# Optimization experiments

Measured on AMD Instinct MI355X. Metric: run time of the kernel, lower is better.

The kernel has to match this reference:

```python
import jax, jax.numpy as jnp
import numpy as np

B, T, S, D, VOCAB = 16, 64, 128, 512, 32000


def setup_inputs():
    key = jax.random.key(0)
    ks = jax.random.split(key, 20)
    w = lambda i, shape: jax.random.normal(ks[i], shape, dtype=jnp.float32) * 0.05
    return {
        'words': jax.random.randint(ks[0], (B, T), 0, VOCAB),
        'encoder_output': jax.random.normal(ks[1], (B, S, D), dtype=jnp.float32),
        'pre_h': jax.random.normal(ks[2], (B, D), dtype=jnp.float32),
        'cell': jax.random.normal(ks[3], (B, D), dtype=jnp.float32),
        'emb': w(4, (VOCAB, D)),
        'W_ih': w(5, (4 * D, D)), 'W_hh': w(6, (4 * D, D)),
        'b_ih': w(7, (4 * D,)), 'b_hh': w(8, (4 * D,)),
        'Wh_w': w(9, (D, D)),
        'Ws_w': w(10, (D, D)), 'Ws_b': w(11, (D,)),
        'vt_w': w(12, (D,)),
        'V_w': w(13, (D, 2 * D)), 'V_b': w(14, (D,)),
        'Vp_w': w(15, (VOCAB, D)), 'Vp_b': w(16, (VOCAB,)),
    }


def lstm(xs, h0, c0, W_ih, W_hh, b_ih, b_hh):
    # xs: [T, B, D]; PyTorch LSTM gate order: i, f, g, o
    def step(carry, x_t):
        h, c = carry
        g = x_t @ W_ih.T + b_ih + h @ W_hh.T + b_hh
        i, f, gg, o = jnp.split(g, 4, axis=-1)
        c = jax.nn.sigmoid(f) * c + jax.nn.sigmoid(i) * jnp.tanh(gg)
        h = jax.nn.sigmoid(o) * jnp.tanh(c)
        return (h, c), h
    _, hs = jax.lax.scan(step, (h0, c0), xs)
    return hs


def reference(words, encoder_output, pre_h, cell, emb, W_ih, W_hh, b_ih, b_hh,
              Wh_w, Ws_w, Ws_b, vt_w, V_w, V_b, Vp_w, Vp_b):
    x = emb[words]                                   # [B, T, D]
    hs = lstm(x.transpose(1, 0, 2), pre_h, cell, W_ih, W_hh, b_ih, b_hh)
    out = hs.transpose(1, 0, 2)                      # [B, T, D] decoder states
    wh = encoder_output @ Wh_w.T                     # [B, S, D]
    ws = out @ Ws_w.T + Ws_b                         # [B, T, D]
    # Bahdanau additive attention scores e[b,s,t] = v_t . tanh(wh[b,s] + ws[b,t])
    e = jnp.einsum('bstd,d->bst', jnp.tanh(wh[:, :, None, :] + ws[:, None, :, :]), vt_w)
    a = jax.nn.softmax(e, axis=1)                    # softmax over source positions
    context = jnp.einsum('bst,bsd->btd', a, encoder_output)
    cat = jnp.concatenate([context, out], axis=-1)   # [B, T, 2D]
    return (cat @ V_w.T + V_b) @ Vp_w.T + Vp_b       # [B, T, VOCAB]
```

## Files before the change

### kernel.cpp

```cpp
#include <hip/hip_runtime.h>

#define DEV __device__ __forceinline__

typedef float f32x4 __attribute__((ext_vector_type(4)));
typedef short s16x8 __attribute__((ext_vector_type(8)));
typedef unsigned short u16;
typedef u16 u16x4 __attribute__((ext_vector_type(4)));
typedef u16 u16x8 __attribute__((ext_vector_type(8)));
typedef unsigned int u32x4 __attribute__((ext_vector_type(4)));

constexpr int Bb = 16, Tt = 64, Ss = 128, Dd = 512, Vv = 32000, FD = 2048;

DEV u16 f2bf(float x) {
  unsigned u = __builtin_bit_cast(unsigned, x);
  u = u + 0x7fffu + ((u >> 16) & 1u);
  return (u16)(u >> 16);
}
DEV float bf2f(u16 h) { unsigned u = ((unsigned)h) << 16; return __builtin_bit_cast(float, u); }
DEV float sigm(float x) { return 1.f / (1.f + __expf(-x)); }
DEV float ftanh(float x) {
  x = fminf(15.f, fmaxf(-15.f, x));
  float e = __expf(2.f * x);
  return (e - 1.f) / (e + 1.f);
}

DEV void cvt_plain_one(const float* __restrict__ in, u16* __restrict__ out, int i) {
  float4 v = reinterpret_cast<const float4*>(in)[i];
  u16x4 o;
  o.x = f2bf(v.x); o.y = f2bf(v.y); o.z = f2bf(v.z); o.w = f2bf(v.w);
  reinterpret_cast<u16x4*>(out)[i] = o;
}

DEV void cvt_split_one(const float* __restrict__ in, u16* __restrict__ hi,
                       u16* __restrict__ lo, int i) {
  float4 v = reinterpret_cast<const float4*>(in)[i];
  u16x4 oh, ol;
  float vv[4] = {v.x, v.y, v.z, v.w};
#pragma unroll
  for (int j = 0; j < 4; ++j) {
    u16 h = f2bf(vv[j]);
    oh[j] = h;
    ol[j] = f2bf(vv[j] - bf2f(h));
  }
  reinterpret_cast<u16x4*>(hi)[i] = oh;
  reinterpret_cast<u16x4*>(lo)[i] = ol;
}

__global__ void k_pre(const int* __restrict__ words, const float* __restrict__ emb,
                      u16* __restrict__ xb,
                      const float* __restrict__ pre, unsigned* __restrict__ hp0,
                      const float* __restrict__ bi, const float* __restrict__ bh,
                      float* __restrict__ bsum,
                      const float* __restrict__ Wih, u16* __restrict__ Wih_bf,
                      const float* __restrict__ enc, u16* __restrict__ ench,
                      u16* __restrict__ encl,
                      const float* __restrict__ Whw, u16* __restrict__ whh,
                      u16* __restrict__ whl) {
  int blk = blockIdx.x, tid = threadIdx.x;
  if (blk < Bb * Tt) {
    int row = words[blk];
    int d = tid * 2;
    float2 v = *reinterpret_cast<const float2*>(&emb[(size_t)row * Dd + d]);
    xb[(size_t)blk * Dd + d] = f2bf(v.x);
    xb[(size_t)blk * Dd + d + 1] = f2bf(v.y);
  } else if (blk < Bb * Tt + 32) {
    int i = (blk - Bb * Tt) * 256 + tid;
    float v = pre[i];
    u16 h = f2bf(v);
    u16 l = f2bf(v - bf2f(h));
    hp0[i] = (unsigned)h | ((unsigned)l << 16);
  } else if (blk < Bb * Tt + 40) {
    int i = (blk - Bb * Tt - 32) * 256 + tid;
    bsum[i] = bi[i] + bh[i];
  } else {
    const int n0 = FD * Dd / 4, n1 = Bb * Ss * Dd / 4, n2 = Dd * Dd / 4;
    int total = n0 + n1 + n2;
    int i = (blk - (Bb * Tt + 40)) * 256 + tid;
    int st = 256 * 256;
    for (; i < total; i += st) {
      if (i < n0) cvt_plain_one(Wih, Wih_bf, i);
      else if (i < n0 + n1) cvt_split_one(enc, ench, encl, i - n0);
      else cvt_split_one(Whw, whh, whl, i - n0 - n1);
    }
  }
}

template <bool BIAS, bool OUTBF, int TERMS>
DEV void gemm_body(u16* ls, int tile, int tid,
                   const u16* __restrict__ A, const u16* __restrict__ Al,
                   const u16* __restrict__ Bm, const u16* __restrict__ Bl,
                   float* __restrict__ Cf, u16* __restrict__ Cb,
                   const float* __restrict__ bias, int M, int N, int K) {
  u16* lsA = ls;
  u16* lsB = ls + 128 * 32;
  u16* lsAl = ls + 2 * 128 * 32;
  u16* lsBl = ls + 3 * 128 * 32;
  const int mt = M >> 7;
  const int tm = (tile % mt) << 7;
  const int tn = (tile / mt) << 7;
  const int wave = tid >> 6, lane = tid & 63;
  const int wr = wave >> 1, wc = wave & 1;
  f32x4 acc[4][4];
#pragma unroll
  for (int i = 0; i < 4; ++i)
#pragma unroll
    for (int j = 0; j < 4; ++j) acc[i][j] = (f32x4){0.f, 0.f, 0.f, 0.f};

  const int lrow = lane >> 2;
  const int lk = (lane & 3) << 3;
  const int fr = lane & 15, fk = (lane >> 4) << 3;

  for (int k0 = 0; k0 < K; k0 += 32) {
#pragma unroll
    for (int r = 0; r < 2; ++r) {
      int rowA = r * 64 + wave * 16;
      size_t goffA = (size_t)(tm + rowA + lrow) * K + k0 + lk;
      size_t goffB = (size_t)(tn + rowA + lrow) * K + k0 + lk;
      __builtin_amdgcn_global_load_lds((const __attribute__((address_space(1))) void*)(A + goffA),
                                       (__attribute__((address_space(3))) void*)&lsA[rowA * 32],
                                       16, 0, 0);
      __builtin_amdgcn_global_load_lds((const __attribute__((address_space(1))) void*)(Bm + goffB),
                                       (__attribute__((address_space(3))) void*)&lsB[rowA * 32],
                                       16, 0, 0);
      if constexpr (TERMS == 3) {
        __builtin_amdgcn_global_load_lds((const __attribute__((address_space(1))) void*)(Al + goffA),
                                         (__attribute__((address_space(3))) void*)&lsAl[rowA * 32],
                                         16, 0, 0);
        __builtin_amdgcn_global_load_lds((const __attribute__((address_space(1))) void*)(Bl + goffB),
                                         (__attribute__((address_space(3))) void*)&lsBl[rowA * 32],
                                         16, 0, 0);
      }
    }
    __syncthreads();
    s16x8 av[4], bv[4];
#pragma unroll
    for (int mi = 0; mi < 4; ++mi)
      av[mi] = *reinterpret_cast<const s16x8*>(&lsA[(wr * 64 + mi * 16 + fr) * 32 + fk]);
#pragma unroll
    for (int ni = 0; ni < 4; ++ni)
      bv[ni] = *reinterpret_cast<const s16x8*>(&lsB[(wc * 64 + ni * 16 + fr) * 32 + fk]);
    if constexpr (TERMS == 3) {
      s16x8 avl[4], bvl[4];
#pragma unroll
      for (int mi = 0; mi < 4; ++mi)
        avl[mi] = *reinterpret_cast<const s16x8*>(&lsAl[(wr * 64 + mi * 16 + fr) * 32 + fk]);
#pragma unroll
      for (int ni = 0; ni < 4; ++ni)
        bvl[ni] = *reinterpret_cast<const s16x8*>(&lsBl[(wc * 64 + ni * 16 + fr) * 32 + fk]);
#pragma unroll
      for (int mi = 0; mi < 4; ++mi)
#pragma unroll
        for (int ni = 0; ni < 4; ++ni) {
          acc[mi][ni] = __builtin_amdgcn_mfma_f32_16x16x32_bf16(av[mi], bv[ni], acc[mi][ni], 0, 0, 0);
          acc[mi][ni] = __builtin_amdgcn_mfma_f32_16x16x32_bf16(av[mi], bvl[ni], acc[mi][ni], 0, 0, 0);
          acc[mi][ni] = __builtin_amdgcn_mfma_f32_16x16x32_bf16(avl[mi], bv[ni], acc[mi][ni], 0, 0, 0);
        }
    } else {
#pragma unroll
      for (int mi = 0; mi < 4; ++mi)
#pragma unroll
        for (int ni = 0; ni < 4; ++ni)
          acc[mi][ni] = __builtin_amdgcn_mfma_f32_16x16x32_bf16(av[mi], bv[ni], acc[mi][ni], 0, 0, 0);
    }
    __syncthreads();
  }

  const int fm = (lane >> 4) << 2;
#pragma unroll
  for (int ni = 0; ni < 4; ++ni) {
    int col = tn + wc * 64 + ni * 16 + fr;
    float badd = 0.f;
    if constexpr (BIAS) badd = bias[col];
#pragma unroll
    for (int mi = 0; mi < 4; ++mi) {
#pragma unroll
      for (int r = 0; r < 4; ++r) {
        int row = tm + wr * 64 + mi * 16 + fm + r;
        size_t idx = (size_t)row * N + col;
        float v = acc[mi][ni][r] + badd;
        if constexpr (OUTBF) Cb[idx] = f2bf(v);
        else Cf[idx] = v;
      }
    }
  }
}

template <bool BIAS, bool OUTBF, int TERMS>
__global__ __launch_bounds__(256) void k_gemm(const u16* __restrict__ A,
                                              const u16* __restrict__ Al,
                                              const u16* __restrict__ Bm,
                                              const u16* __restrict__ Bl,
                                              float* __restrict__ Cf, u16* __restrict__ Cb,
                                              const float* __restrict__ bias,
                                              int M, int N, int K) {
  __shared__ u16 ls[4 * 128 * 32];
  gemm_body<BIAS, OUTBF, TERMS>(ls, blockIdx.x, threadIdx.x, A, Al, Bm, Bl, Cf, Cb, bias, M, N, K);
}

__global__ __launch_bounds__(256) void k_logits_sw(const u16* __restrict__ hmid,
                                                   const u16* __restrict__ Vp_bf,
                                                   const float* __restrict__ Vp_b,
                                                   float* __restrict__ outp) {
  __shared__ u16 ls[4 * 128 * 32];
  const int id = blockIdx.x;
  const int n = (id & 7) + 8 * (id >> 6);
  const int m = (id >> 3) & 7;
  if (n >= 250) return;
  gemm_body<true, false, 1>(ls, n * 8 + m, threadIdx.x, hmid, nullptr, Vp_bf, nullptr,
                            outp, nullptr, Vp_b, 1024, 32000, 512);
}

DEV void lstm_body(int w, int tid, float* gls,
                   const float* __restrict__ xg, const float* __restrict__ Whh,
                   const float* __restrict__ cell, unsigned* __restrict__ hpack,
                   u16* __restrict__ out_hi, u16* __restrict__ out_lo,
                   int* __restrict__ flags) {
  const int gi = tid >> 6, lane = tid & 63;
  const int ds0 = w << 4;
  float (*g_lds)[16][16] = (float(*)[16][16])gls;

  const int fr = lane & 15;
  const int fkb = (lane >> 4) << 3;

  s16x8 whi[16], wlo[16];
  {
    const float* wrow = Whh + (size_t)(gi * Dd + ds0 + fr) * Dd;
#pragma unroll
    for (int kc = 0; kc < 16; ++kc) {
      int k = kc * 32 + fkb;
      float4 a = *reinterpret_cast<const float4*>(&wrow[k]);
      float4 b = *reinterpret_cast<const float4*>(&wrow[k + 4]);
      float vv[8] = {a.x, a.y, a.z, a.w, b.x, b.y, b.z, b.w};
#pragma unroll
      for (int j = 0; j < 8; ++j) {
        u16 h = f2bf(vv[j]);
        whi[kc][j] = (short)h;
        wlo[kc][j] = (short)f2bf(vv[j] - bf2f(h));
      }
    }
  }

  const int ub = tid >> 4, ud = tid & 15;
  float c = cell[(size_t)ub * Dd + ds0 + ud];

  for (int t = 0; t < Tt; ++t) {
    float xgv[4];
#pragma unroll
    for (int r = 0; r < 4; ++r) {
      int bb = ((lane >> 4) << 2) + r;
      xgv[r] = xg[(size_t)(bb * Tt + t) * FD + gi * Dd + ds0 + fr];
    }
#pragma unroll
    for (int r = 0; r < 4; ++r) asm volatile("" ::"v"(xgv[r]));

    if (t > 0) {
      if (gi == 0) {
        if (lane < 32 && lane != w) {
          while (__hip_atomic_load(&flags[lane * 32], __ATOMIC_RELAXED,
                                   __HIP_MEMORY_SCOPE_AGENT) < t) {}
          while (__hip_atomic_load(&flags[lane * 32], __ATOMIC_ACQUIRE,
                                   __HIP_MEMORY_SCOPE_AGENT) < t) {}
        }
        __builtin_amdgcn_sched_barrier(0);
      }
      __syncthreads();
    }

    const unsigned* hp = hpack + (size_t)t * (Bb * Dd) + (size_t)fr * Dd;
    f32x4 a0 = (f32x4){0.f, 0.f, 0.f, 0.f};
    f32x4 a1 = a0, a2 = a0;
#pragma unroll
    for (int kc = 0; kc < 16; ++kc) {
      int k = kc * 32 + fkb;
      u32x4 u0 = *reinterpret_cast<const u32x4*>(&hp[k]);
      u32x4 u1 = *reinterpret_cast<const u32x4*>(&hp[k + 4]);
      s16x8 ahi, alo;
#pragma unroll
      for (int j = 0; j < 4; ++j) {
        ahi[j] = (short)(u0[j] & 0xffffu); alo[j] = (short)(u0[j] >> 16);
        ahi[4 + j] = (short)(u1[j] & 0xffffu); alo[4 + j] = (short)(u1[j] >> 16);
      }
      a0 = __builtin_amdgcn_mfma_f32_16x16x32_bf16(ahi, whi[kc], a0, 0, 0, 0);
      a1 = __builtin_amdgcn_mfma_f32_16x16x32_bf16(ahi, wlo[kc], a1, 0, 0, 0);
      a2 = __builtin_amdgcn_mfma_f32_16x16x32_bf16(alo, whi[kc], a2, 0, 0, 0);
    }
#pragma unroll
    for (int r = 0; r < 4; ++r) {
      int bb = ((lane >> 4) << 2) + r;
      g_lds[gi][bb][fr] = a0[r] + a1[r] + a2[r] + xgv[r];
    }
    __syncthreads();
    float iv = g_lds[0][ub][ud], fv = g_lds[1][ub][ud];
    float gv = g_lds[2][ub][ud], ov = g_lds[3][ub][ud];
    c = sigm(fv) * c + sigm(iv) * ftanh(gv);
    float h = sigm(ov) * ftanh(c);
    u16 hh = f2bf(h);
    u16 hl = f2bf(h - bf2f(hh));
    unsigned pk = (unsigned)hh | ((unsigned)hl << 16);
    __hip_atomic_store(&hpack[(size_t)(t + 1) * (Bb * Dd) + ub * Dd + ds0 + ud], pk,
                       __ATOMIC_RELAXED, __HIP_MEMORY_SCOPE_AGENT);
    size_t oidx = (size_t)(ub * Tt + t) * Dd + ds0 + ud;
    out_hi[oidx] = hh;
    out_lo[oidx] = hl;
    __syncthreads();
    if (tid == 0)
      __hip_atomic_store(&flags[w * 32], t + 1, __ATOMIC_RELAXED, __HIP_MEMORY_SCOPE_AGENT);
  }
}

__global__ __launch_bounds__(256) void k_lstm_fused(
    const float* __restrict__ xg, const float* __restrict__ Whh,
    const float* __restrict__ cell, unsigned* __restrict__ hpack,
    u16* __restrict__ out_hi, u16* __restrict__ out_lo, int* __restrict__ flags,
    const u16* __restrict__ enc_hi, const u16* __restrict__ enc_lo,
    const u16* __restrict__ Whw_hi, const u16* __restrict__ Whw_lo,
    float* __restrict__ wh,
    const float* __restrict__ Vp_w, u16* __restrict__ Vp_bf,
    const float* __restrict__ V_w, u16* __restrict__ Vw_bf,
    const float* __restrict__ Ws_w, u16* __restrict__ Wsw_hi, u16* __restrict__ Wsw_lo) {
  __shared__ u16 ls[4 * 128 * 32];
  const int blk = blockIdx.x, tid = threadIdx.x;
  if (blk < 32) {
    lstm_body(blk, tid, (float*)ls, xg, Whh, cell, hpack, out_hi, out_lo, flags);
  } else if (blk < 96) {
    gemm_body<false, false, 3>(ls, blk - 32, tid, enc_hi, enc_lo, Whw_hi, Whw_lo,
                               wh, nullptr, nullptr, 2048, 512, 512);
  } else {
    const int nVp = Vv * Dd / 4, nV = Dd * 2 * Dd / 4, nWs = Dd * Dd / 4;
    int total = nVp + nV + nWs;
    int i = (blk - 96) * 256 + tid;
    int st = 160 * 256;
    for (; i < total; i += st) {
      if (i < nVp) cvt_plain_one(Vp_w, Vp_bf, i);
      else if (i < nVp + nV) cvt_plain_one(V_w, Vw_bf, i - nVp);
      else cvt_split_one(Ws_w, Wsw_hi, Wsw_lo, i - nVp - nV);
    }
  }
}

__global__ __launch_bounds__(256) void k_attn(const float* __restrict__ wh,
                                              const float* __restrict__ wst,
                                              const float* __restrict__ vt,
                                              const float* __restrict__ enc,
                                              const u16* __restrict__ out_hi,
                                              u16* __restrict__ cat) {
  const int tid = threadIdx.x;
  const int wave = tid >> 6, lane = tid & 63;
  const int wid = blockIdx.x * 4 + wave;
  const int b = wid >> 6, t = wid & 63;
  const int d0 = lane << 3;

  float wsv[8], vtv[8];
  {
    const float4* p = reinterpret_cast<const float4*>(&wst[(size_t)(b * Tt + t) * Dd + d0]);
    float4 x = p[0], y = p[1];
    wsv[0] = x.x; wsv[1] = x.y; wsv[2] = x.z; wsv[3] = x.w;
    wsv[4] = y.x; wsv[5] = y.y; wsv[6] = y.z; wsv[7] = y.w;
    const float4* q = reinterpret_cast<const float4*>(&vt[d0]);
    float4 u = q[0], v = q[1];
    vtv[0] = u.x; vtv[1] = u.y; vtv[2] = u.z; vtv[3] = u.w;
    vtv[4] = v.x; vtv[5] = v.y; vtv[6] = v.z; vtv[7] = v.w;
  }
  float e0 = 0.f, e1 = 0.f;
  for (int s = 0; s < Ss; ++s) {
    const float4* p = reinterpret_cast<const float4*>(&wh[(size_t)(b * Ss + s) * Dd + d0]);
    float4 x = p[0], y = p[1];
    float whv[8] = {x.x, x.y, x.z, x.w, y.x, y.y, y.z, y.w};
    float a = 0.f;
#pragma unroll
    for (int j = 0; j < 8; ++j) a += ftanh(whv[j] + wsv[j]) * vtv[j];
#pragma unroll
    for (int off = 32; off; off >>= 1) a += __shfl_xor(a, off);
    if (lane == (s & 63)) { if (s < 64) e0 = a; else e1 = a; }
  }
  float m = fmaxf(e0, e1);
#pragma unroll
  for (int off = 32; off; off >>= 1) m = fmaxf(m, __shfl_xor(m, off));
  float p0 = __expf(e0 - m), p1 = __expf(e1 - m);
  float sum = p0 + p1;
#pragma unroll
  for (int off = 32; off; off >>= 1) sum += __shfl_xor(sum, off);
  float inv = 1.f / sum;
  float a0 = p0 * inv, a1 = p1 * inv;

  float ctx[8] = {0.f, 0.f, 0.f, 0.f, 0.f, 0.f, 0.f, 0.f};
  for (int s = 0; s < Ss; ++s) {
    float as = __shfl(s < 64 ? a0 : a1, s & 63);
    const float4* p = reinterpret_cast<const float4*>(&enc[(size_t)(b * Ss + s) * Dd + d0]);
    float4 x = p[0], y = p[1];
    ctx[0] += as * x.x; ctx[1] += as * x.y; ctx[2] += as * x.z; ctx[3] += as * x.w;
    ctx[4] += as * y.x; ctx[5] += as * y.y; ctx[6] += as * y.z; ctx[7] += as * y.w;
  }
  u16x8 co;
#pragma unroll
  for (int j = 0; j < 8; ++j) co[j] = f2bf(ctx[j]);
  size_t cbase = (size_t)(b * Tt + t) * (2 * Dd);
  *reinterpret_cast<u16x8*>(&cat[cbase + d0]) = co;
  u16x8 ov = *reinterpret_cast<const u16x8*>(&out_hi[(size_t)(b * Tt + t) * Dd + d0]);
  *reinterpret_cast<u16x8*>(&cat[cbase + Dd + d0]) = ov;
}

extern "C" void kernel_launch(void* const* d_in, const int* in_sizes, int n_in,
                              void* d_out, int out_size, void* d_ws, size_t ws_size,
                              hipStream_t stream) {
  const int* words = (const int*)d_in[0];
  const float* enc = (const float*)d_in[1];
  const float* pre_h = (const float*)d_in[2];
  const float* cell = (const float*)d_in[3];
  const float* emb = (const float*)d_in[4];
  const float* W_ih = (const float*)d_in[5];
  const float* W_hh = (const float*)d_in[6];
  const float* b_ih = (const float*)d_in[7];
  const float* b_hh = (const float*)d_in[8];
  const float* Wh_w = (const float*)d_in[9];
  const float* Ws_w = (const float*)d_in[10];
  const float* Ws_b = (const float*)d_in[11];
  const float* vt_w = (const float*)d_in[12];
  const float* V_w = (const float*)d_in[13];
  const float* V_b = (const float*)d_in[14];
  const float* Vp_w = (const float*)d_in[15];
  const float* Vp_b = (const float*)d_in[16];
  float* outp = (float*)d_out;

  char* ws = (char*)d_ws;
  size_t off = 0;
  auto alloc = [&](size_t bytes) {
    char* p = ws + off;
    off = (off + bytes + 255) & ~(size_t)255;
    return p;
  };
  int* flags = (int*)alloc(4096);
  float* xg = (float*)alloc((size_t)Bb * Tt * FD * 4);
  float* wh = (float*)alloc((size_t)Bb * Ss * Dd * 4);
  float* wst = (float*)alloc((size_t)Bb * Tt * Dd * 4);
  unsigned* hpack = (unsigned*)alloc((size_t)(Tt + 1) * Bb * Dd * 4);
  u16* out_hi = (u16*)alloc((size_t)Bb * Tt * Dd * 2);
  u16* out_lo = (u16*)alloc((size_t)Bb * Tt * Dd * 2);
  u16* x_bf = (u16*)alloc((size_t)Bb * Tt * Dd * 2);
  u16* enc_hi = (u16*)alloc((size_t)Bb * Ss * Dd * 2);
  u16* enc_lo = (u16*)alloc((size_t)Bb * Ss * Dd * 2);
  u16* Wih_bf = (u16*)alloc((size_t)FD * Dd * 2);
  u16* Whw_hi = (u16*)alloc((size_t)Dd * Dd * 2);
  u16* Whw_lo = (u16*)alloc((size_t)Dd * Dd * 2);
  u16* Wsw_hi = (u16*)alloc((size_t)Dd * Dd * 2);
  u16* Wsw_lo = (u16*)alloc((size_t)Dd * Dd * 2);
  u16* Vw_bf = (u16*)alloc((size_t)Dd * 2 * Dd * 2);
  u16* Vp_bf = (u16*)alloc((size_t)Vv * Dd * 2);
  u16* cat = (u16*)alloc((size_t)Bb * Tt * 2 * Dd * 2);
  u16* hmid = (u16*)alloc((size_t)Bb * Tt * Dd * 2);
  float* bsum = (float*)alloc((size_t)FD * 4);
  if (off > ws_size) return;

  hipMemsetAsync(flags, 0, 4096, stream);

  k_pre<<<Bb * Tt + 40 + 256, 256, 0, stream>>>(words, emb, x_bf, pre_h, (unsigned*)hpack,
                                                b_ih, b_hh, bsum,
                                                W_ih, Wih_bf, enc, enc_hi, enc_lo,
                                                Wh_w, Whw_hi, Whw_lo);
  k_gemm<true, false, 1><<<8 * 16, 256, 0, stream>>>(x_bf, nullptr, Wih_bf, nullptr,
                                                     xg, nullptr, bsum, 1024, 2048, 512);
  k_lstm_fused<<<256, 256, 0, stream>>>(xg, W_hh, cell, (unsigned*)hpack, out_hi, out_lo,
                                        flags, enc_hi, enc_lo, Whw_hi, Whw_lo, wh,
                                        Vp_w, Vp_bf, V_w, Vw_bf, Ws_w, Wsw_hi, Wsw_lo);
  k_gemm<true, false, 3><<<8 * 4, 256, 0, stream>>>(out_hi, out_lo, Wsw_hi, Wsw_lo,
                                                    wst, nullptr, Ws_b, 1024, 512, 512);
  k_attn<<<256, 256, 0, stream>>>(wh, wst, vt_w, enc, out_hi, cat);
  k_gemm<true, true, 1><<<8 * 4, 256, 0, stream>>>(cat, nullptr, Vw_bf, nullptr,
                                                   nullptr, hmid, V_b, 1024, 512, 1024);
  k_logits_sw<<<2048, 256, 0, stream>>>(hmid, Vp_bf, Vp_b, outp);
}
```

Baseline: 581.6 us.

## Fuse Ws projection, attention, and V projection into one tail kernel

Replaces three launches (the Ws GEMM, the attention kernel and the V GEMM) with a single k_tail kernel. Each block handles 8 decoder rows of one batch element. It computes ws with MFMA into shared memory, runs additive attention to build the concatenated context row in shared memory, then applies V_w via MFMA and writes hmid. This removes two launch gaps and the global round-trips of wst and cat. In exchange it uses only 128 blocks, wastes half of each 16-row MFMA tile, and has every block re-read the full Ws and V weights.

```diff
diff --git a/kernel.cpp b/kernel.cpp
--- a/kernel.cpp
+++ b/kernel.cpp
@@ -338,66 +338,135 @@
   }
 }
 
-__global__ __launch_bounds__(256) void k_attn(const float* __restrict__ wh,
-                                              const float* __restrict__ wst,
-                                              const float* __restrict__ vt,
-                                              const float* __restrict__ enc,
-                                              const u16* __restrict__ out_hi,
-                                              u16* __restrict__ cat) {
-  const int tid = threadIdx.x;
-  const int wave = tid >> 6, lane = tid & 63;
-  const int wid = blockIdx.x * 4 + wave;
-  const int b = wid >> 6, t = wid & 63;
-  const int d0 = lane << 3;
-
-  float wsv[8], vtv[8];
+__global__ __launch_bounds__(256) void k_tail(
+    const u16* __restrict__ out_hi, const u16* __restrict__ out_lo,
+    const u16* __restrict__ Wsw_hi, const u16* __restrict__ Wsw_lo,
+    const float* __restrict__ Ws_b,
+    const float* __restrict__ wh, const float* __restrict__ vt,
+    const float* __restrict__ enc,
+    const u16* __restrict__ Vw_bf, const float* __restrict__ V_b,
+    u16* __restrict__ hmid) {
+  __shared__ float ws_s[8][Dd];
+  __shared__ u16 cat_s[8][2 * Dd];
+  const int blk = blockIdx.x, tid = threadIdx.x;
+  const int b = blk >> 3, tc = blk & 7;
+  const int wv = tid >> 6, lane = tid & 63;
+  const int fr = lane & 15, fkb = (lane >> 4) << 3;
+
   {
-    const float4* p = reinterpret_cast<const float4*>(&wst[(size_t)(b * Tt + t) * Dd + d0]);
-    float4 x = p[0], y = p[1];
-    wsv[0] = x.x; wsv[1] = x.y; wsv[2] = x.z; wsv[3] = x.w;
-    wsv[4] = y.x; wsv[5] = y.y; wsv[6] = y.z; wsv[7] = y.w;
-    const float4* q = reinterpret_cast<const float4*>(&vt[d0]);
-    float4 u = q[0], v = q[1];
-    vtv[0] = u.x; vtv[1] = u.y; vtv[2] = u.z; vtv[3] = u.w;
-    vtv[4] = v.x; vtv[5] = v.y; vtv[6] = v.z; vtv[7] = v.w;
-  }
-  float e0 = 0.f, e1 = 0.f;
-  for (int s = 0; s < Ss; ++s) {
-    const float4* p = reinterpret_cast<const float4*>(&wh[(size_t)(b * Ss + s) * Dd + d0]);
-    float4 x = p[0], y = p[1];
-    float whv[8] = {x.x, x.y, x.z, x.w, y.x, y.y, y.z, y.w};
-    float a = 0.f;
-#pragma unroll
-    for (int j = 0; j < 8; ++j) a += ftanh(whv[j] + wsv[j]) * vtv[j];
-#pragma unroll
-    for (int off = 32; off; off >>= 1) a += __shfl_xor(a, off);
-    if (lane == (s & 63)) { if (s < 64) e0 = a; else e1 = a; }
-  }
-  float m = fmaxf(e0, e1);
-#pragma unroll
-  for (int off = 32; off; off >>= 1) m = fmaxf(m, __shfl_xor(m, off));
-  float p0 = __expf(e0 - m), p1 = __expf(e1 - m);
-  float sum = p0 + p1;
-#pragma unroll
-  for (int off = 32; off; off >>= 1) sum += __shfl_xor(sum, off);
-  float inv = 1.f / sum;
-  float a0 = p0 * inv, a1 = p1 * inv;
-
-  float ctx[8] = {0.f, 0.f, 0.f, 0.f, 0.f, 0.f, 0.f, 0.f};
-  for (int s = 0; s < Ss; ++s) {
-    float as = __shfl(s < 64 ? a0 : a1, s & 63);
-    const float4* p = reinterpret_cast<const float4*>(&enc[(size_t)(b * Ss + s) * Dd + d0]);
-    float4 x = p[0], y = p[1];
-    ctx[0] += as * x.x; ctx[1] += as * x.y; ctx[2] += as * x.z; ctx[3] += as * x.w;
-    ctx[4] += as * y.x; ctx[5] += as * y.y; ctx[6] += as * y.z; ctx[7] += as * y.w;
-  }
-  u16x8 co;
-#pragma unroll
-  for (int j = 0; j < 8; ++j) co[j] = f2bf(ctx[j]);
-  size_t cbase = (size_t)(b * Tt + t) * (2 * Dd);
-  *reinterpret_cast<u16x8*>(&cat[cbase + d0]) = co;
-  u16x8 ov = *reinterpret_cast<const u16x8*>(&out_hi[(size_t)(b * Tt + t) * Dd + d0]);
-  *reinterpret_cast<u16x8*>(&cat[cbase + Dd + d0]) = ov;
+    f32x4 acc8[8];
+#pragma unroll
+    for (int n = 0; n < 8; ++n) acc8[n] = (f32x4){0.f, 0.f, 0.f, 0.f};
+    const int j = fr & 7;
+    const size_t arow = (size_t)(b * Tt + tc * 8 + j) * Dd;
+    for (int kc = 0; kc < 16; ++kc) {
+      int k = kc * 32 + fkb;
+      s16x8 ah = *reinterpret_cast<const s16x8*>(&out_hi[arow + k]);
+      s16x8 al = *reinterpret_cast<const s16x8*>(&out_lo[arow + k]);
+#pragma unroll
+      for (int n = 0; n < 8; ++n) {
+        size_t brow = (size_t)(wv * 128 + n * 16 + fr) * Dd + k;
+        s16x8 bh = *reinterpret_cast<const s16x8*>(&Wsw_hi[brow]);
+        s16x8 bl = *reinterpret_cast<const s16x8*>(&Wsw_lo[brow]);
+        acc8[n] = __builtin_amdgcn_mfma_f32_16x16x32_bf16(ah, bh, acc8[n], 0, 0, 0);
+        acc8[n] = __builtin_amdgcn_mfma_f32_16x16x32_bf16(ah, bl, acc8[n], 0, 0, 0);
+        acc8[n] = __builtin_amdgcn_mfma_f32_16x16x32_bf16(al, bh, acc8[n], 0, 0, 0);
+      }
+    }
+#pragma unroll
+    for (int n = 0; n < 8; ++n) {
+      int col = wv * 128 + n * 16 + fr;
+      float badd = Ws_b[col];
+#pragma unroll
+      for (int r = 0; r < 4; ++r) {
+        int row = (lane >> 4) * 4 + r;
+        if (row < 8) ws_s[row][col] = acc8[n][r] + badd;
+      }
+    }
+  }
+  __syncthreads();
+
+  {
+    const int d0 = lane << 3;
+    float vtv[8];
+    {
+      const float4* q = reinterpret_cast<const float4*>(&vt[d0]);
+      float4 u = q[0], v = q[1];
+      vtv[0] = u.x; vtv[1] = u.y; vtv[2] = u.z; vtv[3] = u.w;
+      vtv[4] = v.x; vtv[5] = v.y; vtv[6] = v.z; vtv[7] = v.w;
+    }
+    for (int rr = 0; rr < 2; ++rr) {
+      int j = wv * 2 + rr;
+      float wsv[8];
+#pragma unroll
+      for (int d = 0; d < 8; ++d) wsv[d] = ws_s[j][d0 + d];
+      float e0 = 0.f, e1 = 0.f;
+      for (int s = 0; s < Ss; ++s) {
+        const float4* p = reinterpret_cast<const float4*>(&wh[(size_t)(b * Ss + s) * Dd + d0]);
+        float4 x = p[0], y = p[1];
+        float whv[8] = {x.x, x.y, x.z, x.w, y.x, y.y, y.z, y.w};
+        float a = 0.f;
+#pragma unroll
+        for (int d = 0; d < 8; ++d) a += ftanh(whv[d] + wsv[d]) * vtv[d];
+#pragma unroll
+        for (int off = 32; off; off >>= 1) a += __shfl_xor(a, off);
+        if (lane == (s & 63)) { if (s < 64) e0 = a; else e1 = a; }
+      }
+      float m = fmaxf(e0, e1);
+#pragma unroll
+      for (int off = 32; off; off >>= 1) m = fmaxf(m, __shfl_xor(m, off));
+      float p0 = __expf(e0 - m), p1 = __expf(e1 - m);
+      float sum = p0 + p1;
+#pragma unroll
+      for (int off = 32; off; off >>= 1) sum += __shfl_xor(sum, off);
+      float inv = 1.f / sum;
+      float a0s = p0 * inv, a1s = p1 * inv;
+      float ctx[8] = {0.f, 0.f, 0.f, 0.f, 0.f, 0.f, 0.f, 0.f};
+      for (int s = 0; s < Ss; ++s) {
+        float as = __shfl(s < 64 ? a0s : a1s, s & 63);
+        const float4* p = reinterpret_cast<const float4*>(&enc[(size_t)(b * Ss + s) * Dd + d0]);
+        float4 x = p[0], y = p[1];
+        ctx[0] += as * x.x; ctx[1] += as * x.y; ctx[2] += as * x.z; ctx[3] += as * x.w;
+        ctx[4] += as * y.x; ctx[5] += as * y.y; ctx[6] += as * y.z; ctx[7] += as * y.w;
+      }
+      u16x8 co;
+#pragma unroll
+      for (int d = 0; d < 8; ++d) co[d] = f2bf(ctx[d]);
+      *reinterpret_cast<u16x8*>(&cat_s[j][d0]) = co;
+      size_t orow = (size_t)(b * Tt + tc * 8 + j) * Dd;
+      u16x8 ov = *reinterpret_cast<const u16x8*>(&out_hi[orow + d0]);
+      *reinterpret_cast<u16x8*>(&cat_s[j][Dd + d0]) = ov;
+    }
+  }
+  __syncthreads();
+
+  {
+    f32x4 acc8[8];
+#pragma unroll
+    for (int n = 0; n < 8; ++n) acc8[n] = (f32x4){0.f, 0.f, 0.f, 0.f};
+    const int j = fr & 7;
+    for (int kc = 0; kc < 32; ++kc) {
+      int k = kc * 32 + fkb;
+      s16x8 a = *reinterpret_cast<const s16x8*>(&cat_s[j][k]);
+#pragma unroll
+      for (int n = 0; n < 8; ++n) {
+        size_t brow = (size_t)(wv * 128 + n * 16 + fr) * (2 * Dd) + k;
+        s16x8 bf = *reinterpret_cast<const s16x8*>(&Vw_bf[brow]);
+        acc8[n] = __builtin_amdgcn_mfma_f32_16x16x32_bf16(a, bf, acc8[n], 0, 0, 0);
+      }
+    }
+#pragma unroll
+    for (int n = 0; n < 8; ++n) {
+      int col = wv * 128 + n * 16 + fr;
+      float badd = V_b[col];
+#pragma unroll
+      for (int r = 0; r < 4; ++r) {
+        int row = (lane >> 4) * 4 + r;
+        if (row < 8)
+          hmid[(size_t)(b * Tt + tc * 8 + row) * Dd + col] = f2bf(acc8[n][r] + badd);
+      }
+    }
+  }
 }
 
 extern "C" void kernel_launch(void* const* d_in, const int* in_sizes, int n_in,
@@ -432,7 +501,6 @@
   int* flags = (int*)alloc(4096);
   float* xg = (float*)alloc((size_t)Bb * Tt * FD * 4);
   float* wh = (float*)alloc((size_t)Bb * Ss * Dd * 4);
-  float* wst = (float*)alloc((size_t)Bb * Tt * Dd * 4);
   unsigned* hpack = (unsigned*)alloc((size_t)(Tt + 1) * Bb * Dd * 4);
   u16* out_hi = (u16*)alloc((size_t)Bb * Tt * Dd * 2);
   u16* out_lo = (u16*)alloc((size_t)Bb * Tt * Dd * 2);
@@ -446,7 +514,6 @@
   u16* Wsw_lo = (u16*)alloc((size_t)Dd * Dd * 2);
   u16* Vw_bf = (u16*)alloc((size_t)Dd * 2 * Dd * 2);
   u16* Vp_bf = (u16*)alloc((size_t)Vv * Dd * 2);
-  u16* cat = (u16*)alloc((size_t)Bb * Tt * 2 * Dd * 2);
   u16* hmid = (u16*)alloc((size_t)Bb * Tt * Dd * 2);
   float* bsum = (float*)alloc((size_t)FD * 4);
   if (off > ws_size) return;
@@ -462,10 +529,7 @@
   k_lstm_fused<<<256, 256, 0, stream>>>(xg, W_hh, cell, (unsigned*)hpack, out_hi, out_lo,
                                         flags, enc_hi, enc_lo, Whw_hi, Whw_lo, wh,
                                         Vp_w, Vp_bf, V_w, Vw_bf, Ws_w, Wsw_hi, Wsw_lo);
-  k_gemm<true, false, 3><<<8 * 4, 256, 0, stream>>>(out_hi, out_lo, Wsw_hi, Wsw_lo,
-                                                    wst, nullptr, Ws_b, 1024, 512, 512);
-  k_attn<<<256, 256, 0, stream>>>(wh, wst, vt_w, enc, out_hi, cat);
-  k_gemm<true, true, 1><<<8 * 4, 256, 0, stream>>>(cat, nullptr, Vw_bf, nullptr,
-                                                   nullptr, hmid, V_b, 1024, 512, 1024);
+  k_tail<<<128, 256, 0, stream>>>(out_hi, out_lo, Wsw_hi, Wsw_lo, Ws_b,
+                                  wh, vt_w, enc, Vw_bf, V_b, hmid);
   k_logits_sw<<<2048, 256, 0, stream>>>(hmid, Vp_bf, Vp_b, outp);
 }
```

Result: slower. 717.9 us (+23.4%).
